# Optimization experiments

Hardware: AMD Instinct MI355X
Metric: run time of the kernel (lower is better)

The kernel has to match this reference:

```python
import jax, jax.numpy as jnp
import numpy as np

# Static problem sizes (uniform complexes so the per-complex torch loop vectorizes)
B, P, L = 8, 512, 64          # complexes, protein atoms/complex, ligand atoms/complex
H, RB = 128, 32               # hidden_dim, radial_bins
CUTOFF = 8.0
NPT, NLT = 20, 16             # atom-type vocab sizes


def _linear_init(k, din, dout):
    s = 1.0 / np.sqrt(din)
    kw, kb = jax.random.split(k)
    W = jax.random.uniform(kw, (din, dout), minval=-s, maxval=s, dtype=jnp.float32)
    b = jax.random.uniform(kb, (dout,), minval=-s, maxval=s, dtype=jnp.float32)
    return W, b


def setup_inputs() -> dict:
    key = jax.random.key(0)
    ks = jax.random.split(key, 12)
    # positions spread over ~a pocket-sized box so the cutoff mask is non-trivial
    protein_pos = jax.random.normal(ks[0], (B * P, 3), dtype=jnp.float32) * 4.0
    ligand_pos = jax.random.normal(ks[1], (B * L, 3), dtype=jnp.float32) * 4.0
    protein_atom_type = jax.random.randint(ks[2], (B * P,), 0, NPT)
    ligand_atom_type = jax.random.randint(ks[3], (B * L,), 0, NLT)
    protein_batch = jnp.repeat(jnp.arange(B), P)
    ligand_batch = jnp.repeat(jnp.arange(B), L)
    prot_emb = jax.random.normal(ks[4], (NPT, H), dtype=jnp.float32)
    lig_emb = jax.random.normal(ks[5], (NLT, H), dtype=jnp.float32)
    W1, b1 = _linear_init(ks[6], 2 * H + RB, H)
    W2, b2 = _linear_init(ks[7], H, H)
    W3, b3 = _linear_init(ks[8], H, H)
    Wr1, br1 = _linear_init(ks[9], H, H)
    Wr2, br2 = _linear_init(ks[10], H, 1)
    return dict(protein_pos=protein_pos, ligand_pos=ligand_pos,
                prot_emb=prot_emb, lig_emb=lig_emb,
                W1=W1, b1=b1, W2=W2, b2=b2, W3=W3, b3=b3,
                Wr1=Wr1, br1=br1, Wr2=Wr2, br2=br2,
                protein_atom_type=protein_atom_type, ligand_atom_type=ligand_atom_type,
                protein_batch=protein_batch, ligand_batch=ligand_batch)


def reference(protein_pos, ligand_pos, prot_emb, lig_emb,
              W1, b1, W2, b2, W3, b3, Wr1, br1, Wr2, br2,
              protein_atom_type, ligand_atom_type, protein_batch, ligand_batch):
    # batches are contiguous with uniform P/L atoms per complex -> reshape to [B, ., .]
    pos_p = protein_pos.reshape(B, P, 3)
    pos_l = ligand_pos.reshape(B, L, 3)
    hp = prot_emb[protein_atom_type].reshape(B, P, H)
    hl = lig_emb[ligand_atom_type].reshape(B, L, H)

    diff = pos_p[:, :, None, :] - pos_l[:, None, :, :]          # [B,P,L,3]
    dist = jnp.linalg.norm(diff, axis=-1)                        # [B,P,L]
    mask = dist < CUTOFF                                         # [B,P,L]

    centers = jnp.linspace(0.0, CUTOFF, RB, dtype=dist.dtype)    # radial_centers buffer
    width = jnp.asarray(0.5 * CUTOFF / RB, dtype=dist.dtype)     # radial_width buffer
    rb = jnp.exp(-0.5 * ((dist[..., None] - centers) / (width + 1e-8)) ** 2)  # [B,P,L,RB]

    pair = jnp.concatenate([
        jnp.broadcast_to(hp[:, :, None, :], (B, P, L, H)),
        jnp.broadcast_to(hl[:, None, :, :], (B, P, L, H)),
        rb,
    ], axis=-1)                                                  # [B,P,L,2H+RB]

    h = jax.nn.relu(pair @ W1 + b1)
    h = jax.nn.relu(h @ W2 + b2)
    h = jax.nn.relu(h @ W3 + b3)                                 # [B,P,L,H]

    m = mask[..., None].astype(h.dtype)
    cnt = jnp.sum(mask, axis=(1, 2)).astype(h.dtype)             # valid pairs per complex
    complex_repr = jnp.sum(h * m, axis=(1, 2)) / jnp.maximum(cnt, 1.0)[:, None]  # [B,H]

    score = jax.nn.relu(complex_repr @ Wr1 + br1) @ Wr2 + br2    # [B,1]
    score = jnp.where(cnt[:, None] > 0, score, 0.0)              # torch emits 0 if no pairs
    return score[:, 0]                                           # [B]
```

## Files before the change

kernel.cpp:

```cpp
#include <hip/hip_runtime.h>
#include <hip/hip_bf16.h>
#include <math.h>

#define NB 8
#define NP 512
#define NL 64
#define NH 128
#define NRB 32
#define NPT 20
#define NLT 16
#define PAIRS_CAP (NP * NL)
#define CHUNKS 512
#define K1 96

typedef __attribute__((ext_vector_type(8))) _Float16 h8;
typedef __attribute__((ext_vector_type(4))) float f4;

__global__ __launch_bounds__(256) void prep(
    const float* __restrict__ ppos, const float* __restrict__ lpos,
    const int* __restrict__ ptype_g, const int* __restrict__ ltype_g,
    const float* __restrict__ pemb, const float* __restrict__ lemb,
    const float* __restrict__ W1, const float* __restrict__ b1,
    const float* __restrict__ W2, const float* __restrict__ W3,
    uint2* __restrict__ rec, unsigned* __restrict__ cnt,
    _Float16* __restrict__ wt1e, _Float16* __restrict__ wt2t,
    _Float16* __restrict__ wt3t, float* __restrict__ acc)
{
  int blk = blockIdx.x, tid = threadIdx.x;

  if (blk < 8) {
    int b = blk;
    int w = tid >> 6, lane = tid & 63;
    __shared__ float slig[NL * 3];
    __shared__ int slt[NL];
    __shared__ unsigned wtot[4];

    if (tid < NL * 3) slig[tid] = lpos[b * NL * 3 + tid];
    if (tid < NL) slt[tid] = ltype_g[b * NL + tid];
    __syncthreads();

    const float* pp = ppos + (size_t)(b * NP + 2 * tid) * 3;
    float p0x = pp[0], p0y = pp[1], p0z = pp[2];
    float p1x = pp[3], p1y = pp[4], p1z = pp[5];
    unsigned pt0 = (unsigned)ptype_g[b * NP + 2 * tid];
    unsigned pt1 = (unsigned)ptype_g[b * NP + 2 * tid + 1];

    unsigned long long m0 = 0ull, m1 = 0ull;
    for (int l = 0; l < NL; ++l) {
      float qx = slig[3 * l + 0], qy = slig[3 * l + 1], qz = slig[3 * l + 2];
      float dx0 = p0x - qx, dy0 = p0y - qy, dz0 = p0z - qz;
      float dx1 = p1x - qx, dy1 = p1y - qy, dz1 = p1z - qz;
      bool v0 = sqrtf(dx0 * dx0 + dy0 * dy0 + dz0 * dz0) < 8.0f;
      bool v1 = sqrtf(dx1 * dx1 + dy1 * dy1 + dz1 * dz1) < 8.0f;
      m0 |= ((unsigned long long)v0) << l;
      m1 |= ((unsigned long long)v1) << l;
    }
    unsigned count = (unsigned)(__popcll(m0) + __popcll(m1));

    unsigned inc = count;
    #pragma unroll
    for (int d = 1; d < 64; d <<= 1) {
      unsigned v = __shfl_up(inc, d);
      if (lane >= d) inc += v;
    }
    if (lane == 63) wtot[w] = inc;
    __syncthreads();
    unsigned wbase = 0;
    for (int i = 0; i < w; ++i) wbase += wtot[i];
    unsigned base = wbase + inc - count;
    if (tid == 255) cnt[b] = wbase + inc;

    uint2* dst = rec + (size_t)b * PAIRS_CAP;
    unsigned long long mm = m0;
    while (mm) {
      int l = __builtin_ctzll(mm); mm &= mm - 1ull;
      float dx = p0x - slig[3 * l], dy = p0y - slig[3 * l + 1], dz = p0z - slig[3 * l + 2];
      float d = sqrtf(dx * dx + dy * dy + dz * dz);
      dst[base++] = (uint2){__float_as_uint(d), (pt0 << 16) | (unsigned)slt[l]};
    }
    mm = m1;
    while (mm) {
      int l = __builtin_ctzll(mm); mm &= mm - 1ull;
      float dx = p1x - slig[3 * l], dy = p1y - slig[3 * l + 1], dz = p1z - slig[3 * l + 2];
      float d = sqrtf(dx * dx + dy * dy + dz * dz);
      dst[base++] = (uint2){__float_as_uint(d), (pt1 << 16) | (unsigned)slt[l]};
    }
    return;
  }

  if (blk == 8) {
    for (int i = tid; i < NB * NH; i += 256) acc[i] = 0.0f;
    return;
  }

  if (blk < 105) {
    int k = blk - 9;
    if (tid >= NH) return;
    int c = tid;
    float v;
    if (k < 32) {
      v = W1[(2 * NH + k) * NH + c];
    } else if (k < 52) {
      int t = k - 32;
      float s = b1[c];
      for (int j = 0; j < NH; ++j)
        s = fmaf(pemb[t * NH + j], W1[j * NH + c], s);
      v = s;
    } else if (k < 68) {
      int t = k - 52;
      float s = 0.0f;
      for (int j = 0; j < NH; ++j)
        s = fmaf(lemb[t * NH + j], W1[(NH + j) * NH + c], s);
      v = s;
    } else {
      v = 0.0f;
    }
    wt1e[c * K1 + k] = (_Float16)v;
    return;
  }

  {
    int k = blk - 105;
    if (tid >= NH) return;
    int c = tid;
    wt2t[c * NH + k] = (_Float16)W2[k * NH + c];
    wt3t[c * NH + k] = (_Float16)W3[k * NH + c];
    return;
  }
}

__device__ __forceinline__ int swz(int row, int col) {
  return row * NH + (col ^ ((row & 7) << 3));
}

__global__ __launch_bounds__(256, 4) void pair_mlp(
    const _Float16* __restrict__ wt1e, const _Float16* __restrict__ wt2t,
    const _Float16* __restrict__ wt3t,
    const float* __restrict__ b2, const float* __restrict__ b3,
    const uint2* __restrict__ rec, const unsigned* __restrict__ cnt,
    float* __restrict__ accum)
{
  __shared__ _Float16 sA[NL * NH];
  __shared__ _Float16 sB[NL * NH];

  int tid = threadIdx.x;
  int cg = __builtin_amdgcn_readfirstlane(tid >> 6);
  int l  = tid & 63;
  int b     = blockIdx.x & 7;
  int chunk = blockIdx.x >> 3;

  unsigned total = cnt[b];
  if ((unsigned)(chunk * 64) >= total) return;

  int idx = chunk * 64 + l;
  int src = ((unsigned)idx < total) ? idx : 0;
  uint2 rcd = rec[(size_t)b * PAIRS_CAP + src];
  float dist = __uint_as_float(rcd.x);
  int pt = (int)(rcd.y >> 16), lt = (int)(rcd.y & 0xffffu);

  const float stepc = 8.0f / 31.0f;
  const float invw = 1.0f / (0.125f + 1e-8f);

  for (int jj = 0; jj < 3; ++jj) {
    int ch = 3 * cg + jj;
    h8 v;
    #pragma unroll
    for (int i = 0; i < 8; ++i) {
      int c = ch * 8 + i;
      float x;
      if (c < 32) { float t = (dist - stepc * (float)c) * invw; x = __expf(-0.5f * t * t); }
      else if (c < 52) x = (c - 32 == pt) ? 1.0f : 0.0f;
      else if (c < 68) x = (c - 52 == lt) ? 1.0f : 0.0f;
      else x = 0.0f;
      v[i] = (_Float16)x;
    }
    *(h8*)&sB[swz(l, ch * 8)] = v;
  }
  __syncthreads();

  int col0 = cg * 32 + (l & 15);
  int krow = 8 * (l >> 4);
  int g4 = (l >> 4) * 4;

  {
    h8 B1[2][3];
    #pragma unroll
    for (int n = 0; n < 2; ++n)
      #pragma unroll
      for (int kk = 0; kk < 3; ++kk)
        B1[n][kk] = *(const h8*)&wt1e[(col0 + 16 * n) * K1 + 32 * kk + krow];

    f4 acc1[4][2];
    #pragma unroll
    for (int m = 0; m < 4; ++m)
      #pragma unroll
      for (int n = 0; n < 2; ++n)
        acc1[m][n] = (f4){0.0f, 0.0f, 0.0f, 0.0f};

    #pragma unroll
    for (int m = 0; m < 4; ++m) {
      int row = 16 * m + (l & 15);
      #pragma unroll
      for (int kk = 0; kk < 3; ++kk) {
        h8 a = *(const h8*)&sB[swz(row, 32 * kk + krow)];
        acc1[m][0] = __builtin_amdgcn_mfma_f32_16x16x32_f16(a, B1[0][kk], acc1[m][0], 0, 0, 0);
        acc1[m][1] = __builtin_amdgcn_mfma_f32_16x16x32_f16(a, B1[1][kk], acc1[m][1], 0, 0, 0);
      }
    }
    #pragma unroll
    for (int m = 0; m < 4; ++m)
      #pragma unroll
      for (int n = 0; n < 2; ++n)
        #pragma unroll
        for (int r = 0; r < 4; ++r) {
          int row = 16 * m + g4 + r;
          sA[swz(row, cg * 32 + 16 * n + (l & 15))] =
              (_Float16)fmaxf(acc1[m][n][r], 0.0f);
        }
  }
  __syncthreads();

  {
    h8 B2[2][4];
    #pragma unroll
    for (int n = 0; n < 2; ++n)
      #pragma unroll
      for (int kk = 0; kk < 4; ++kk)
        B2[n][kk] = *(const h8*)&wt2t[(col0 + 16 * n) * NH + 32 * kk + krow];

    float bias0 = b2[col0], bias1 = b2[col0 + 16];
    f4 acc2[4][2];
    #pragma unroll
    for (int m = 0; m < 4; ++m) {
      acc2[m][0] = (f4){bias0, bias0, bias0, bias0};
      acc2[m][1] = (f4){bias1, bias1, bias1, bias1};
    }
    #pragma unroll
    for (int m = 0; m < 4; ++m) {
      int row = 16 * m + (l & 15);
      #pragma unroll
      for (int kk = 0; kk < 4; ++kk) {
        h8 a = *(const h8*)&sA[swz(row, 32 * kk + krow)];
        acc2[m][0] = __builtin_amdgcn_mfma_f32_16x16x32_f16(a, B2[0][kk], acc2[m][0], 0, 0, 0);
        acc2[m][1] = __builtin_amdgcn_mfma_f32_16x16x32_f16(a, B2[1][kk], acc2[m][1], 0, 0, 0);
      }
    }
    __syncthreads();
    #pragma unroll
    for (int m = 0; m < 4; ++m)
      #pragma unroll
      for (int n = 0; n < 2; ++n)
        #pragma unroll
        for (int r = 0; r < 4; ++r) {
          int row = 16 * m + g4 + r;
          sB[swz(row, cg * 32 + 16 * n + (l & 15))] =
              (_Float16)fmaxf(acc2[m][n][r], 0.0f);
        }
  }
  __syncthreads();

  {
    h8 B3[2][4];
    #pragma unroll
    for (int n = 0; n < 2; ++n)
      #pragma unroll
      for (int kk = 0; kk < 4; ++kk)
        B3[n][kk] = *(const h8*)&wt3t[(col0 + 16 * n) * NH + 32 * kk + krow];

    float bias0 = b3[col0], bias1 = b3[col0 + 16];
    f4 acc3[4][2];
    #pragma unroll
    for (int m = 0; m < 4; ++m) {
      acc3[m][0] = (f4){bias0, bias0, bias0, bias0};
      acc3[m][1] = (f4){bias1, bias1, bias1, bias1};
    }
    #pragma unroll
    for (int m = 0; m < 4; ++m) {
      int row = 16 * m + (l & 15);
      #pragma unroll
      for (int kk = 0; kk < 4; ++kk) {
        h8 a = *(const h8*)&sB[swz(row, 32 * kk + krow)];
        acc3[m][0] = __builtin_amdgcn_mfma_f32_16x16x32_f16(a, B3[0][kk], acc3[m][0], 0, 0, 0);
        acc3[m][1] = __builtin_amdgcn_mfma_f32_16x16x32_f16(a, B3[1][kk], acc3[m][1], 0, 0, 0);
      }
    }

    int rem = (int)total - chunk * 64;
    float cs0 = 0.0f, cs1 = 0.0f;
    #pragma unroll
    for (int m = 0; m < 4; ++m)
      #pragma unroll
      for (int r = 0; r < 4; ++r) {
        int row = 16 * m + g4 + r;
        bool ok = row < rem;
        cs0 += ok ? fmaxf(acc3[m][0][r], 0.0f) : 0.0f;
        cs1 += ok ? fmaxf(acc3[m][1][r], 0.0f) : 0.0f;
      }
    cs0 += __shfl_xor(cs0, 16); cs0 += __shfl_xor(cs0, 32);
    cs1 += __shfl_xor(cs1, 16); cs1 += __shfl_xor(cs1, 32);
    int g = l >> 4;
    if (g == 0)      atomicAdd(&accum[b * NH + cg * 32 + (l & 15)], cs0);
    else if (g == 1) atomicAdd(&accum[b * NH + cg * 32 + 16 + (l & 15)], cs1);
  }
}

__global__ __launch_bounds__(128) void score_head(
    const float* __restrict__ acc, const unsigned* __restrict__ cnt,
    const float* __restrict__ Wr1, const float* __restrict__ br1,
    const float* __restrict__ Wr2, const float* __restrict__ br2,
    float* __restrict__ out)
{
  int b = blockIdx.x;
  int tid = threadIdx.x;
  __shared__ float sr[NH];
  __shared__ float wsum[2];
  unsigned c = cnt[b];
  float denom = fmaxf((float)c, 1.0f);
  sr[tid] = acc[b * NH + tid] / denom;
  __syncthreads();
  float s = br1[tid];
  for (int k = 0; k < NH; ++k)
    s = fmaf(sr[k], Wr1[k * NH + tid], s);
  float v = fmaxf(s, 0.0f) * Wr2[tid];
  #pragma unroll
  for (int d = 1; d < 64; d <<= 1) v += __shfl_xor(v, d);
  if ((tid & 63) == 0) wsum[tid >> 6] = v;
  __syncthreads();
  if (tid == 0)
    out[b] = (c > 0) ? (wsum[0] + wsum[1] + br2[0]) : 0.0f;
}

extern "C" void kernel_launch(void* const* d_in, const int* in_sizes, int n_in,
                              void* d_out, int out_size, void* d_ws, size_t ws_size,
                              hipStream_t stream)
{
  const float* ppos = (const float*)d_in[0];
  const float* lpos = (const float*)d_in[1];
  const float* pemb = (const float*)d_in[2];
  const float* lemb = (const float*)d_in[3];
  const float* W1   = (const float*)d_in[4];
  const float* b1   = (const float*)d_in[5];
  const float* W2   = (const float*)d_in[6];
  const float* b2   = (const float*)d_in[7];
  const float* W3   = (const float*)d_in[8];
  const float* b3   = (const float*)d_in[9];
  const float* Wr1  = (const float*)d_in[10];
  const float* br1  = (const float*)d_in[11];
  const float* Wr2  = (const float*)d_in[12];
  const float* br2  = (const float*)d_in[13];
  const int*   ptyp = (const int*)d_in[14];
  const int*   ltyp = (const int*)d_in[15];

  float* ws  = (float*)d_ws;
  float* acc = ws;
  unsigned* cnt = (unsigned*)(ws + 1024);
  uint2* rec = (uint2*)(ws + 1032);
  _Float16* wt1e = (_Float16*)(ws + 1032 + 524288);
  _Float16* wt2t = (_Float16*)(ws + 1032 + 524288 + 6144);
  _Float16* wt3t = (_Float16*)(ws + 1032 + 524288 + 6144 + 8192);

  prep<<<233, 256, 0, stream>>>(ppos, lpos, ptyp, ltyp, pemb, lemb,
                                W1, b1, W2, W3,
                                rec, cnt, wt1e, wt2t, wt3t, acc);
  pair_mlp<<<NB * CHUNKS, 256, 0, stream>>>(wt1e, wt2t, wt3t, b2, b3,
                                            rec, cnt, acc);
  score_head<<<NB, 128, 0, stream>>>(acc, cnt, Wr1, br1, Wr2, br2, (float*)d_out);
}
```

Measured before the change: 57.72 us.

## Give each wave its own 16-row pair tile, dropping inter-wave barriers

```diff
diff --git a/kernel.cpp b/kernel.cpp
--- a/kernel.cpp
+++ b/kernel.cpp
@@ -130,7 +130,7 @@
 }
 
 __device__ __forceinline__ int swz(int row, int col) {
-  return row * NH + (col ^ ((row & 7) << 3));
+  return row * NH + (col ^ ((row & 15) << 3));
 }
 
 __global__ __launch_bounds__(256, 4) void pair_mlp(
@@ -140,11 +140,11 @@
     const uint2* __restrict__ rec, const unsigned* __restrict__ cnt,
     float* __restrict__ accum)
 {
-  __shared__ _Float16 sA[NL * NH];
-  __shared__ _Float16 sB[NL * NH];
+  __shared__ _Float16 sS[NL * NH];
+  __shared__ float comb[4 * NH];
 
   int tid = threadIdx.x;
-  int cg = __builtin_amdgcn_readfirstlane(tid >> 6);
+  int w  = __builtin_amdgcn_readfirstlane(tid >> 6);
   int l  = tid & 63;
   int b     = blockIdx.x & 7;
   int chunk = blockIdx.x >> 3;
@@ -152,7 +152,11 @@
   unsigned total = cnt[b];
   if ((unsigned)(chunk * 64) >= total) return;
 
-  int idx = chunk * 64 + l;
+  int c16  = l & 15;
+  int g    = l >> 4;
+  int row0 = 16 * w;
+
+  int idx = chunk * 64 + row0 + c16;
   int src = ((unsigned)idx < total) ? idx : 0;
   uint2 rcd = rec[(size_t)b * PAIRS_CAP + src];
   float dist = __uint_as_float(rcd.x);
@@ -161,146 +165,114 @@
   const float stepc = 8.0f / 31.0f;
   const float invw = 1.0f / (0.125f + 1e-8f);
 
-  for (int jj = 0; jj < 3; ++jj) {
-    int ch = 3 * cg + jj;
-    h8 v;
-    #pragma unroll
-    for (int i = 0; i < 8; ++i) {
-      int c = ch * 8 + i;
-      float x;
-      if (c < 32) { float t = (dist - stepc * (float)c) * invw; x = __expf(-0.5f * t * t); }
-      else if (c < 52) x = (c - 32 == pt) ? 1.0f : 0.0f;
-      else if (c < 68) x = (c - 52 == lt) ? 1.0f : 0.0f;
-      else x = 0.0f;
-      v[i] = (_Float16)x;
-    }
-    *(h8*)&sB[swz(l, ch * 8)] = v;
-  }
-  __syncthreads();
-
-  int col0 = cg * 32 + (l & 15);
-  int krow = 8 * (l >> 4);
-  int g4 = (l >> 4) * 4;
+  h8 a1k0, a1k1, a1k2;
+  #pragma unroll
+  for (int j = 0; j < 8; ++j) {
+    int u = 8 * g + j;
+    float t = (dist - stepc * (float)u) * invw;
+    a1k0[j] = (_Float16)__expf(-0.5f * t * t);
+    a1k1[j] = (_Float16)((u < 20) ? ((u == pt) ? 1.0f : 0.0f)
+                                  : ((u - 20 == lt) ? 1.0f : 0.0f));
+    a1k2[j] = (_Float16)(((u < 4) && (u + 12 == lt)) ? 1.0f : 0.0f);
+  }
+
+  f4 acc[8];
+  #pragma unroll
+  for (int nn = 0; nn < 8; ++nn) acc[nn] = (f4){0.0f, 0.0f, 0.0f, 0.0f};
+  #pragma unroll
+  for (int nn = 0; nn < 8; ++nn) {
+    const _Float16* wp = &wt1e[(16 * nn + c16) * K1 + 8 * g];
+    h8 bf0 = *(const h8*)&wp[0];
+    h8 bf1 = *(const h8*)&wp[32];
+    h8 bf2 = *(const h8*)&wp[64];
+    acc[nn] = __builtin_amdgcn_mfma_f32_16x16x32_f16(a1k0, bf0, acc[nn], 0, 0, 0);
+    acc[nn] = __builtin_amdgcn_mfma_f32_16x16x32_f16(a1k1, bf1, acc[nn], 0, 0, 0);
+    acc[nn] = __builtin_amdgcn_mfma_f32_16x16x32_f16(a1k2, bf2, acc[nn], 0, 0, 0);
+  }
+  #pragma unroll
+  for (int nn = 0; nn < 8; ++nn)
+    #pragma unroll
+    for (int r = 0; r < 4; ++r)
+      sS[swz(row0 + 4 * g + r, 16 * nn + c16)] = (_Float16)fmaxf(acc[nn][r], 0.0f);
 
   {
-    h8 B1[2][3];
-    #pragma unroll
-    for (int n = 0; n < 2; ++n)
+    h8 a0 = *(const h8*)&sS[swz(row0 + c16, 8 * g)];
+    h8 a1 = *(const h8*)&sS[swz(row0 + c16, 32 + 8 * g)];
+    h8 a2 = *(const h8*)&sS[swz(row0 + c16, 64 + 8 * g)];
+    h8 a3 = *(const h8*)&sS[swz(row0 + c16, 96 + 8 * g)];
+    f4 acc2[8];
+    #pragma unroll
+    for (int nn = 0; nn < 8; ++nn) {
+      float bb = b2[16 * nn + c16];
+      acc2[nn] = (f4){bb, bb, bb, bb};
+    }
+    #pragma unroll
+    for (int nn = 0; nn < 8; ++nn) {
+      const _Float16* wp = &wt2t[(16 * nn + c16) * NH + 8 * g];
+      h8 bf0 = *(const h8*)&wp[0];
+      h8 bf1 = *(const h8*)&wp[32];
+      h8 bf2 = *(const h8*)&wp[64];
+      h8 bf3 = *(const h8*)&wp[96];
+      acc2[nn] = __builtin_amdgcn_mfma_f32_16x16x32_f16(a0, bf0, acc2[nn], 0, 0, 0);
+      acc2[nn] = __builtin_amdgcn_mfma_f32_16x16x32_f16(a1, bf1, acc2[nn], 0, 0, 0);
+      acc2[nn] = __builtin_amdgcn_mfma_f32_16x16x32_f16(a2, bf2, acc2[nn], 0, 0, 0);
+      acc2[nn] = __builtin_amdgcn_mfma_f32_16x16x32_f16(a3, bf3, acc2[nn], 0, 0, 0);
+    }
+    #pragma unroll
+    for (int nn = 0; nn < 8; ++nn)
       #pragma unroll
-      for (int kk = 0; kk < 3; ++kk)
-        B1[n][kk] = *(const h8*)&wt1e[(col0 + 16 * n) * K1 + 32 * kk + krow];
-
-    f4 acc1[4][2];
-    #pragma unroll
-    for (int m = 0; m < 4; ++m)
-      #pragma unroll
-      for (int n = 0; n < 2; ++n)
-        acc1[m][n] = (f4){0.0f, 0.0f, 0.0f, 0.0f};
-
-    #pragma unroll
-    for (int m = 0; m < 4; ++m) {
-      int row = 16 * m + (l & 15);
-      #pragma unroll
-      for (int kk = 0; kk < 3; ++kk) {
-        h8 a = *(const h8*)&sB[swz(row, 32 * kk + krow)];
-        acc1[m][0] = __builtin_amdgcn_mfma_f32_16x16x32_f16(a, B1[0][kk], acc1[m][0], 0, 0, 0);
-        acc1[m][1] = __builtin_amdgcn_mfma_f32_16x16x32_f16(a, B1[1][kk], acc1[m][1], 0, 0, 0);
-      }
-    }
-    #pragma unroll
-    for (int m = 0; m < 4; ++m)
-      #pragma unroll
-      for (int n = 0; n < 2; ++n)
-        #pragma unroll
-        for (int r = 0; r < 4; ++r) {
-          int row = 16 * m + g4 + r;
-          sA[swz(row, cg * 32 + 16 * n + (l & 15))] =
-              (_Float16)fmaxf(acc1[m][n][r], 0.0f);
-        }
-  }
-  __syncthreads();
-
+      for (int r = 0; r < 4; ++r)
+        sS[swz(row0 + 4 * g + r, 16 * nn + c16)] = (_Float16)fmaxf(acc2[nn][r], 0.0f);
+  }
+
+  float cs[8];
   {
-    h8 B2[2][4];
-    #pragma unroll
-    for (int n = 0; n < 2; ++n)
-      #pragma unroll
-      for (int kk = 0; kk < 4; ++kk)
-        B2[n][kk] = *(const h8*)&wt2t[(col0 + 16 * n) * NH + 32 * kk + krow];
-
-    float bias0 = b2[col0], bias1 = b2[col0 + 16];
-    f4 acc2[4][2];
-    #pragma unroll
-    for (int m = 0; m < 4; ++m) {
-      acc2[m][0] = (f4){bias0, bias0, bias0, bias0};
-      acc2[m][1] = (f4){bias1, bias1, bias1, bias1};
-    }
-    #pragma unroll
-    for (int m = 0; m < 4; ++m) {
-      int row = 16 * m + (l & 15);
-      #pragma unroll
-      for (int kk = 0; kk < 4; ++kk) {
-        h8 a = *(const h8*)&sA[swz(row, 32 * kk + krow)];
-        acc2[m][0] = __builtin_amdgcn_mfma_f32_16x16x32_f16(a, B2[0][kk], acc2[m][0], 0, 0, 0);
-        acc2[m][1] = __builtin_amdgcn_mfma_f32_16x16x32_f16(a, B2[1][kk], acc2[m][1], 0, 0, 0);
-      }
-    }
-    __syncthreads();
-    #pragma unroll
-    for (int m = 0; m < 4; ++m)
-      #pragma unroll
-      for (int n = 0; n < 2; ++n)
-        #pragma unroll
-        for (int r = 0; r < 4; ++r) {
-          int row = 16 * m + g4 + r;
-          sB[swz(row, cg * 32 + 16 * n + (l & 15))] =
-              (_Float16)fmaxf(acc2[m][n][r], 0.0f);
-        }
-  }
-  __syncthreads();
-
-  {
-    h8 B3[2][4];
-    #pragma unroll
-    for (int n = 0; n < 2; ++n)
-      #pragma unroll
-      for (int kk = 0; kk < 4; ++kk)
-        B3[n][kk] = *(const h8*)&wt3t[(col0 + 16 * n) * NH + 32 * kk + krow];
-
-    float bias0 = b3[col0], bias1 = b3[col0 + 16];
-    f4 acc3[4][2];
-    #pragma unroll
-    for (int m = 0; m < 4; ++m) {
-      acc3[m][0] = (f4){bias0, bias0, bias0, bias0};
-      acc3[m][1] = (f4){bias1, bias1, bias1, bias1};
-    }
-    #pragma unroll
-    for (int m = 0; m < 4; ++m) {
-      int row = 16 * m + (l & 15);
-      #pragma unroll
-      for (int kk = 0; kk < 4; ++kk) {
-        h8 a = *(const h8*)&sB[swz(row, 32 * kk + krow)];
-        acc3[m][0] = __builtin_amdgcn_mfma_f32_16x16x32_f16(a, B3[0][kk], acc3[m][0], 0, 0, 0);
-        acc3[m][1] = __builtin_amdgcn_mfma_f32_16x16x32_f16(a, B3[1][kk], acc3[m][1], 0, 0, 0);
-      }
-    }
-
+    h8 a0 = *(const h8*)&sS[swz(row0 + c16, 8 * g)];
+    h8 a1 = *(const h8*)&sS[swz(row0 + c16, 32 + 8 * g)];
+    h8 a2 = *(const h8*)&sS[swz(row0 + c16, 64 + 8 * g)];
+    h8 a3 = *(const h8*)&sS[swz(row0 + c16, 96 + 8 * g)];
+    f4 acc3[8];
+    #pragma unroll
+    for (int nn = 0; nn < 8; ++nn) {
+      float bb = b3[16 * nn + c16];
+      acc3[nn] = (f4){bb, bb, bb, bb};
+    }
+    #pragma unroll
+    for (int nn = 0; nn < 8; ++nn) {
+      const _Float16* wp = &wt3t[(16 * nn + c16) * NH + 8 * g];
+      h8 bf0 = *(const h8*)&wp[0];
+      h8 bf1 = *(const h8*)&wp[32];
+      h8 bf2 = *(const h8*)&wp[64];
+      h8 bf3 = *(const h8*)&wp[96];
+      acc3[nn] = __builtin_amdgcn_mfma_f32_16x16x32_f16(a0, bf0, acc3[nn], 0, 0, 0);
+      acc3[nn] = __builtin_amdgcn_mfma_f32_16x16x32_f16(a1, bf1, acc3[nn], 0, 0, 0);
+      acc3[nn] = __builtin_amdgcn_mfma_f32_16x16x32_f16(a2, bf2, acc3[nn], 0, 0, 0);
+      acc3[nn] = __builtin_amdgcn_mfma_f32_16x16x32_f16(a3, bf3, acc3[nn], 0, 0, 0);
+    }
     int rem = (int)total - chunk * 64;
-    float cs0 = 0.0f, cs1 = 0.0f;
-    #pragma unroll
-    for (int m = 0; m < 4; ++m)
+    #pragma unroll
+    for (int nn = 0; nn < 8; ++nn) {
+      float s = 0.0f;
       #pragma unroll
       for (int r = 0; r < 4; ++r) {
-        int row = 16 * m + g4 + r;
-        bool ok = row < rem;
-        cs0 += ok ? fmaxf(acc3[m][0][r], 0.0f) : 0.0f;
-        cs1 += ok ? fmaxf(acc3[m][1][r], 0.0f) : 0.0f;
+        bool ok = (row0 + 4 * g + r) < rem;
+        s += ok ? fmaxf(acc3[nn][r], 0.0f) : 0.0f;
       }
-    cs0 += __shfl_xor(cs0, 16); cs0 += __shfl_xor(cs0, 32);
-    cs1 += __shfl_xor(cs1, 16); cs1 += __shfl_xor(cs1, 32);
-    int g = l >> 4;
-    if (g == 0)      atomicAdd(&accum[b * NH + cg * 32 + (l & 15)], cs0);
-    else if (g == 1) atomicAdd(&accum[b * NH + cg * 32 + 16 + (l & 15)], cs1);
+      s += __shfl_xor(s, 16);
+      s += __shfl_xor(s, 32);
+      cs[nn] = s;
+    }
+  }
+
+  if (g == 0) {
+    #pragma unroll
+    for (int nn = 0; nn < 8; ++nn)
+      comb[w * NH + 16 * nn + c16] = cs[nn];
+  }
+  __syncthreads();
+  if (tid < NH) {
+    float s = comb[tid] + comb[NH + tid] + comb[2 * NH + tid] + comb[3 * NH + tid];
+    atomicAdd(&accum[b * NH + tid], s);
   }
 }
 
```

Measured after the change: 104.1 us. +80.3%, slower.

## Fuse prep, pair MLP and score head into one cooperative persistent kernel

Applied to the files above, without the earlier changes.

```diff
diff --git a/kernel.cpp b/kernel.cpp
--- a/kernel.cpp
+++ b/kernel.cpp
@@ -1,6 +1,9 @@
 #include <hip/hip_runtime.h>
 #include <hip/hip_bf16.h>
+#include <hip/hip_cooperative_groups.h>
 #include <math.h>
+
+namespace cg = cooperative_groups;
 
 #define NB 8
 #define NP 512
@@ -16,24 +19,37 @@
 typedef __attribute__((ext_vector_type(8))) _Float16 h8;
 typedef __attribute__((ext_vector_type(4))) float f4;
 
-__global__ __launch_bounds__(256) void prep(
+__device__ __forceinline__ int swz(int row, int col) {
+  return row * NH + (col ^ ((row & 7) << 3));
+}
+
+__global__ __launch_bounds__(256, 4) void fused(
     const float* __restrict__ ppos, const float* __restrict__ lpos,
     const int* __restrict__ ptype_g, const int* __restrict__ ltype_g,
     const float* __restrict__ pemb, const float* __restrict__ lemb,
     const float* __restrict__ W1, const float* __restrict__ b1,
-    const float* __restrict__ W2, const float* __restrict__ W3,
+    const float* __restrict__ W2, const float* __restrict__ b2,
+    const float* __restrict__ W3, const float* __restrict__ b3,
+    const float* __restrict__ Wr1, const float* __restrict__ br1,
+    const float* __restrict__ Wr2, const float* __restrict__ br2,
     uint2* __restrict__ rec, unsigned* __restrict__ cnt,
     _Float16* __restrict__ wt1e, _Float16* __restrict__ wt2t,
-    _Float16* __restrict__ wt3t, float* __restrict__ acc)
+    _Float16* __restrict__ wt3t, float* __restrict__ accum,
+    float* __restrict__ out)
 {
-  int blk = blockIdx.x, tid = threadIdx.x;
-
-  if (blk < 8) {
-    int b = blk;
+  __shared__ __align__(16) unsigned char smem[2 * NL * NH * 2];
+  _Float16* sA = (_Float16*)smem;
+  _Float16* sB = (_Float16*)(smem + NL * NH * 2);
+
+  cg::grid_group grid = cg::this_grid();
+  int bid = blockIdx.x, tid = threadIdx.x;
+
+  if (bid < 8) {
+    int b = bid;
     int w = tid >> 6, lane = tid & 63;
-    __shared__ float slig[NL * 3];
-    __shared__ int slt[NL];
-    __shared__ unsigned wtot[4];
+    float* slig = (float*)smem;
+    int* slt = (int*)(smem + 768);
+    unsigned* wtot = (unsigned*)(smem + 1024);
 
     if (tid < NL * 3) slig[tid] = lpos[b * NL * 3 + tid];
     if (tid < NL) slt[tid] = ltype_g[b * NL + tid];
@@ -85,249 +101,230 @@
       float d = sqrtf(dx * dx + dy * dy + dz * dz);
       dst[base++] = (uint2){__float_as_uint(d), (pt1 << 16) | (unsigned)slt[l]};
     }
-    return;
+  } else if (bid == 8) {
+    for (int i = tid; i < NB * NH; i += 256) accum[i] = 0.0f;
+  } else if (bid < 105) {
+    int k = bid - 9;
+    if (tid < NH) {
+      int c = tid;
+      float v;
+      if (k < 32) {
+        v = W1[(2 * NH + k) * NH + c];
+      } else if (k < 52) {
+        int t = k - 32;
+        float s = b1[c];
+        for (int j = 0; j < NH; ++j)
+          s = fmaf(pemb[t * NH + j], W1[j * NH + c], s);
+        v = s;
+      } else if (k < 68) {
+        int t = k - 52;
+        float s = 0.0f;
+        for (int j = 0; j < NH; ++j)
+          s = fmaf(lemb[t * NH + j], W1[(NH + j) * NH + c], s);
+        v = s;
+      } else {
+        v = 0.0f;
+      }
+      wt1e[c * K1 + k] = (_Float16)v;
+    }
+  } else if (bid < 233) {
+    int k = bid - 105;
+    if (tid < NH) {
+      int c = tid;
+      wt2t[c * NH + k] = (_Float16)W2[k * NH + c];
+      wt3t[c * NH + k] = (_Float16)W3[k * NH + c];
+    }
   }
 
-  if (blk == 8) {
-    for (int i = tid; i < NB * NH; i += 256) acc[i] = 0.0f;
-    return;
+  grid.sync();
+
+  {
+    int cg_w = __builtin_amdgcn_readfirstlane(tid >> 6);
+    int l  = tid & 63;
+    int col0 = cg_w * 32 + (l & 15);
+    int krow = 8 * (l >> 4);
+    int g4 = (l >> 4) * 4;
+    const float stepc = 8.0f / 31.0f;
+    const float invw = 1.0f / (0.125f + 1e-8f);
+
+    for (int v = bid; v < NB * CHUNKS; v += gridDim.x) {
+      int b = v & 7;
+      int chunk = v >> 3;
+      unsigned total = cnt[b];
+      if ((unsigned)(chunk * 64) >= total) continue;
+
+      __syncthreads();
+
+      int idx = chunk * 64 + l;
+      int src = ((unsigned)idx < total) ? idx : 0;
+      uint2 rcd = rec[(size_t)b * PAIRS_CAP + src];
+      float dist = __uint_as_float(rcd.x);
+      int pt = (int)(rcd.y >> 16), lt = (int)(rcd.y & 0xffffu);
+
+      for (int jj = 0; jj < 3; ++jj) {
+        int ch = 3 * cg_w + jj;
+        h8 vv;
+        #pragma unroll
+        for (int i = 0; i < 8; ++i) {
+          int c = ch * 8 + i;
+          float x;
+          if (c < 32) { float t = (dist - stepc * (float)c) * invw; x = __expf(-0.5f * t * t); }
+          else if (c < 52) x = (c - 32 == pt) ? 1.0f : 0.0f;
+          else if (c < 68) x = (c - 52 == lt) ? 1.0f : 0.0f;
+          else x = 0.0f;
+          vv[i] = (_Float16)x;
+        }
+        *(h8*)&sB[swz(l, ch * 8)] = vv;
+      }
+      __syncthreads();
+
+      {
+        h8 B1[2][3];
+        #pragma unroll
+        for (int n = 0; n < 2; ++n)
+          #pragma unroll
+          for (int kk = 0; kk < 3; ++kk)
+            B1[n][kk] = *(const h8*)&wt1e[(col0 + 16 * n) * K1 + 32 * kk + krow];
+
+        f4 acc1[4][2];
+        #pragma unroll
+        for (int m = 0; m < 4; ++m)
+          #pragma unroll
+          for (int n = 0; n < 2; ++n)
+            acc1[m][n] = (f4){0.0f, 0.0f, 0.0f, 0.0f};
+
+        #pragma unroll
+        for (int m = 0; m < 4; ++m) {
+          int row = 16 * m + (l & 15);
+          #pragma unroll
+          for (int kk = 0; kk < 3; ++kk) {
+            h8 a = *(const h8*)&sB[swz(row, 32 * kk + krow)];
+            acc1[m][0] = __builtin_amdgcn_mfma_f32_16x16x32_f16(a, B1[0][kk], acc1[m][0], 0, 0, 0);
+            acc1[m][1] = __builtin_amdgcn_mfma_f32_16x16x32_f16(a, B1[1][kk], acc1[m][1], 0, 0, 0);
+          }
+        }
+        #pragma unroll
+        for (int m = 0; m < 4; ++m)
+          #pragma unroll
+          for (int n = 0; n < 2; ++n)
+            #pragma unroll
+            for (int r = 0; r < 4; ++r) {
+              int row = 16 * m + g4 + r;
+              sA[swz(row, cg_w * 32 + 16 * n + (l & 15))] =
+                  (_Float16)fmaxf(acc1[m][n][r], 0.0f);
+            }
+      }
+      __syncthreads();
+
+      {
+        h8 B2[2][4];
+        #pragma unroll
+        for (int n = 0; n < 2; ++n)
+          #pragma unroll
+          for (int kk = 0; kk < 4; ++kk)
+            B2[n][kk] = *(const h8*)&wt2t[(col0 + 16 * n) * NH + 32 * kk + krow];
+
+        float bias0 = b2[col0], bias1 = b2[col0 + 16];
+        f4 acc2[4][2];
+        #pragma unroll
+        for (int m = 0; m < 4; ++m) {
+          acc2[m][0] = (f4){bias0, bias0, bias0, bias0};
+          acc2[m][1] = (f4){bias1, bias1, bias1, bias1};
+        }
+        #pragma unroll
+        for (int m = 0; m < 4; ++m) {
+          int row = 16 * m + (l & 15);
+          #pragma unroll
+          for (int kk = 0; kk < 4; ++kk) {
+            h8 a = *(const h8*)&sA[swz(row, 32 * kk + krow)];
+            acc2[m][0] = __builtin_amdgcn_mfma_f32_16x16x32_f16(a, B2[0][kk], acc2[m][0], 0, 0, 0);
+            acc2[m][1] = __builtin_amdgcn_mfma_f32_16x16x32_f16(a, B2[1][kk], acc2[m][1], 0, 0, 0);
+          }
+        }
+        __syncthreads();
+        #pragma unroll
+        for (int m = 0; m < 4; ++m)
+          #pragma unroll
+          for (int n = 0; n < 2; ++n)
+            #pragma unroll
+            for (int r = 0; r < 4; ++r) {
+              int row = 16 * m + g4 + r;
+              sB[swz(row, cg_w * 32 + 16 * n + (l & 15))] =
+                  (_Float16)fmaxf(acc2[m][n][r], 0.0f);
+            }
+      }
+      __syncthreads();
+
+      {
+        h8 B3[2][4];
+        #pragma unroll
+        for (int n = 0; n < 2; ++n)
+          #pragma unroll
+          for (int kk = 0; kk < 4; ++kk)
+            B3[n][kk] = *(const h8*)&wt3t[(col0 + 16 * n) * NH + 32 * kk + krow];
+
+        float bias0 = b3[col0], bias1 = b3[col0 + 16];
+        f4 acc3[4][2];
+        #pragma unroll
+        for (int m = 0; m < 4; ++m) {
+          acc3[m][0] = (f4){bias0, bias0, bias0, bias0};
+          acc3[m][1] = (f4){bias1, bias1, bias1, bias1};
+        }
+        #pragma unroll
+        for (int m = 0; m < 4; ++m) {
+          int row = 16 * m + (l & 15);
+          #pragma unroll
+          for (int kk = 0; kk < 4; ++kk) {
+            h8 a = *(const h8*)&sB[swz(row, 32 * kk + krow)];
+            acc3[m][0] = __builtin_amdgcn_mfma_f32_16x16x32_f16(a, B3[0][kk], acc3[m][0], 0, 0, 0);
+            acc3[m][1] = __builtin_amdgcn_mfma_f32_16x16x32_f16(a, B3[1][kk], acc3[m][1], 0, 0, 0);
+          }
+        }
+
+        int rem = (int)total - chunk * 64;
+        float cs0 = 0.0f, cs1 = 0.0f;
+        #pragma unroll
+        for (int m = 0; m < 4; ++m)
+          #pragma unroll
+          for (int r = 0; r < 4; ++r) {
+            int row = 16 * m + g4 + r;
+            bool ok = row < rem;
+            cs0 += ok ? fmaxf(acc3[m][0][r], 0.0f) : 0.0f;
+            cs1 += ok ? fmaxf(acc3[m][1][r], 0.0f) : 0.0f;
+          }
+        cs0 += __shfl_xor(cs0, 16); cs0 += __shfl_xor(cs0, 32);
+        cs1 += __shfl_xor(cs1, 16); cs1 += __shfl_xor(cs1, 32);
+        int g = l >> 4;
+        if (g == 0)      atomicAdd(&accum[b * NH + cg_w * 32 + (l & 15)], cs0);
+        else if (g == 1) atomicAdd(&accum[b * NH + cg_w * 32 + 16 + (l & 15)], cs1);
+      }
+    }
   }
 
-  if (blk < 105) {
-    int k = blk - 9;
-    if (tid >= NH) return;
-    int c = tid;
-    float v;
-    if (k < 32) {
-      v = W1[(2 * NH + k) * NH + c];
-    } else if (k < 52) {
-      int t = k - 32;
-      float s = b1[c];
-      for (int j = 0; j < NH; ++j)
-        s = fmaf(pemb[t * NH + j], W1[j * NH + c], s);
-      v = s;
-    } else if (k < 68) {
-      int t = k - 52;
-      float s = 0.0f;
-      for (int j = 0; j < NH; ++j)
-        s = fmaf(lemb[t * NH + j], W1[(NH + j) * NH + c], s);
-      v = s;
-    } else {
-      v = 0.0f;
-    }
-    wt1e[c * K1 + k] = (_Float16)v;
-    return;
+  grid.sync();
+
+  if (bid < NB) {
+    int b = bid;
+    float* sr = (float*)smem;
+    float* wsum = (float*)(smem + 512);
+    unsigned c = cnt[b];
+    float denom = fmaxf((float)c, 1.0f);
+    if (tid < NH) sr[tid] = accum[b * NH + tid] / denom;
+    __syncthreads();
+    float vv = 0.0f;
+    if (tid < NH) {
+      float s = br1[tid];
+      for (int k = 0; k < NH; ++k)
+        s = fmaf(sr[k], Wr1[k * NH + tid], s);
+      vv = fmaxf(s, 0.0f) * Wr2[tid];
+    }
+    #pragma unroll
+    for (int d = 1; d < 64; d <<= 1) vv += __shfl_xor(vv, d);
+    if ((tid & 63) == 0) wsum[tid >> 6] = vv;
+    __syncthreads();
+    if (tid == 0)
+      out[b] = (c > 0) ? (wsum[0] + wsum[1] + br2[0]) : 0.0f;
   }
-
-  {
-    int k = blk - 105;
-    if (tid >= NH) return;
-    int c = tid;
-    wt2t[c * NH + k] = (_Float16)W2[k * NH + c];
-    wt3t[c * NH + k] = (_Float16)W3[k * NH + c];
-    return;
-  }
-}
-
-__device__ __forceinline__ int swz(int row, int col) {
-  return row * NH + (col ^ ((row & 7) << 3));
-}
-
-__global__ __launch_bounds__(256, 4) void pair_mlp(
-    const _Float16* __restrict__ wt1e, const _Float16* __restrict__ wt2t,
-    const _Float16* __restrict__ wt3t,
-    const float* __restrict__ b2, const float* __restrict__ b3,
-    const uint2* __restrict__ rec, const unsigned* __restrict__ cnt,
-    float* __restrict__ accum)
-{
-  __shared__ _Float16 sA[NL * NH];
-  __shared__ _Float16 sB[NL * NH];
-
-  int tid = threadIdx.x;
-  int cg = __builtin_amdgcn_readfirstlane(tid >> 6);
-  int l  = tid & 63;
-  int b     = blockIdx.x & 7;
-  int chunk = blockIdx.x >> 3;
-
-  unsigned total = cnt[b];
-  if ((unsigned)(chunk * 64) >= total) return;
-
-  int idx = chunk * 64 + l;
-  int src = ((unsigned)idx < total) ? idx : 0;
-  uint2 rcd = rec[(size_t)b * PAIRS_CAP + src];
-  float dist = __uint_as_float(rcd.x);
-  int pt = (int)(rcd.y >> 16), lt = (int)(rcd.y & 0xffffu);
-
-  const float stepc = 8.0f / 31.0f;
-  const float invw = 1.0f / (0.125f + 1e-8f);
-
-  for (int jj = 0; jj < 3; ++jj) {
-    int ch = 3 * cg + jj;
-    h8 v;
-    #pragma unroll
-    for (int i = 0; i < 8; ++i) {
-      int c = ch * 8 + i;
-      float x;
-      if (c < 32) { float t = (dist - stepc * (float)c) * invw; x = __expf(-0.5f * t * t); }
-      else if (c < 52) x = (c - 32 == pt) ? 1.0f : 0.0f;
-      else if (c < 68) x = (c - 52 == lt) ? 1.0f : 0.0f;
-      else x = 0.0f;
-      v[i] = (_Float16)x;
-    }
-    *(h8*)&sB[swz(l, ch * 8)] = v;
-  }
-  __syncthreads();
-
-  int col0 = cg * 32 + (l & 15);
-  int krow = 8 * (l >> 4);
-  int g4 = (l >> 4) * 4;
-
-  {
-    h8 B1[2][3];
-    #pragma unroll
-    for (int n = 0; n < 2; ++n)
-      #pragma unroll
-      for (int kk = 0; kk < 3; ++kk)
-        B1[n][kk] = *(const h8*)&wt1e[(col0 + 16 * n) * K1 + 32 * kk + krow];
-
-    f4 acc1[4][2];
-    #pragma unroll
-    for (int m = 0; m < 4; ++m)
-      #pragma unroll
-      for (int n = 0; n < 2; ++n)
-        acc1[m][n] = (f4){0.0f, 0.0f, 0.0f, 0.0f};
-
-    #pragma unroll
-    for (int m = 0; m < 4; ++m) {
-      int row = 16 * m + (l & 15);
-      #pragma unroll
-      for (int kk = 0; kk < 3; ++kk) {
-        h8 a = *(const h8*)&sB[swz(row, 32 * kk + krow)];
-        acc1[m][0] = __builtin_amdgcn_mfma_f32_16x16x32_f16(a, B1[0][kk], acc1[m][0], 0, 0, 0);
-        acc1[m][1] = __builtin_amdgcn_mfma_f32_16x16x32_f16(a, B1[1][kk], acc1[m][1], 0, 0, 0);
-      }
-    }
-    #pragma unroll
-    for (int m = 0; m < 4; ++m)
-      #pragma unroll
-      for (int n = 0; n < 2; ++n)
-        #pragma unroll
-        for (int r = 0; r < 4; ++r) {
-          int row = 16 * m + g4 + r;
-          sA[swz(row, cg * 32 + 16 * n + (l & 15))] =
-              (_Float16)fmaxf(acc1[m][n][r], 0.0f);
-        }
-  }
-  __syncthreads();
-
-  {
-    h8 B2[2][4];
-    #pragma unroll
-    for (int n = 0; n < 2; ++n)
-      #pragma unroll
-      for (int kk = 0; kk < 4; ++kk)
-        B2[n][kk] = *(const h8*)&wt2t[(col0 + 16 * n) * NH + 32 * kk + krow];
-
-    float bias0 = b2[col0], bias1 = b2[col0 + 16];
-    f4 acc2[4][2];
-    #pragma unroll
-    for (int m = 0; m < 4; ++m) {
-      acc2[m][0] = (f4){bias0, bias0, bias0, bias0};
-      acc2[m][1] = (f4){bias1, bias1, bias1, bias1};
-    }
-    #pragma unroll
-    for (int m = 0; m < 4; ++m) {
-      int row = 16 * m + (l & 15);
-      #pragma unroll
-      for (int kk = 0; kk < 4; ++kk) {
-        h8 a = *(const h8*)&sA[swz(row, 32 * kk + krow)];
-        acc2[m][0] = __builtin_amdgcn_mfma_f32_16x16x32_f16(a, B2[0][kk], acc2[m][0], 0, 0, 0);
-        acc2[m][1] = __builtin_amdgcn_mfma_f32_16x16x32_f16(a, B2[1][kk], acc2[m][1], 0, 0, 0);
-      }
-    }
-    __syncthreads();
-    #pragma unroll
-    for (int m = 0; m < 4; ++m)
-      #pragma unroll
-      for (int n = 0; n < 2; ++n)
-        #pragma unroll
-        for (int r = 0; r < 4; ++r) {
-          int row = 16 * m + g4 + r;
-          sB[swz(row, cg * 32 + 16 * n + (l & 15))] =
-              (_Float16)fmaxf(acc2[m][n][r], 0.0f);
-        }
-  }
-  __syncthreads();
-
-  {
-    h8 B3[2][4];
-    #pragma unroll
-    for (int n = 0; n < 2; ++n)
-      #pragma unroll
-      for (int kk = 0; kk < 4; ++kk)
-        B3[n][kk] = *(const h8*)&wt3t[(col0 + 16 * n) * NH + 32 * kk + krow];
-
-    float bias0 = b3[col0], bias1 = b3[col0 + 16];
-    f4 acc3[4][2];
-    #pragma unroll
-    for (int m = 0; m < 4; ++m) {
-      acc3[m][0] = (f4){bias0, bias0, bias0, bias0};
-      acc3[m][1] = (f4){bias1, bias1, bias1, bias1};
-    }
-    #pragma unroll
-    for (int m = 0; m < 4; ++m) {
-      int row = 16 * m + (l & 15);
-      #pragma unroll
-      for (int kk = 0; kk < 4; ++kk) {
-        h8 a = *(const h8*)&sB[swz(row, 32 * kk + krow)];
-        acc3[m][0] = __builtin_amdgcn_mfma_f32_16x16x32_f16(a, B3[0][kk], acc3[m][0], 0, 0, 0);
-        acc3[m][1] = __builtin_amdgcn_mfma_f32_16x16x32_f16(a, B3[1][kk], acc3[m][1], 0, 0, 0);
-      }
-    }
-
-    int rem = (int)total - chunk * 64;
-    float cs0 = 0.0f, cs1 = 0.0f;
-    #pragma unroll
-    for (int m = 0; m < 4; ++m)
-      #pragma unroll
-      for (int r = 0; r < 4; ++r) {
-        int row = 16 * m + g4 + r;
-        bool ok = row < rem;
-        cs0 += ok ? fmaxf(acc3[m][0][r], 0.0f) : 0.0f;
-        cs1 += ok ? fmaxf(acc3[m][1][r], 0.0f) : 0.0f;
-      }
-    cs0 += __shfl_xor(cs0, 16); cs0 += __shfl_xor(cs0, 32);
-    cs1 += __shfl_xor(cs1, 16); cs1 += __shfl_xor(cs1, 32);
-    int g = l >> 4;
-    if (g == 0)      atomicAdd(&accum[b * NH + cg * 32 + (l & 15)], cs0);
-    else if (g == 1) atomicAdd(&accum[b * NH + cg * 32 + 16 + (l & 15)], cs1);
-  }
-}
-
-__global__ __launch_bounds__(128) void score_head(
-    const float* __restrict__ acc, const unsigned* __restrict__ cnt,
-    const float* __restrict__ Wr1, const float* __restrict__ br1,
-    const float* __restrict__ Wr2, const float* __restrict__ br2,
-    float* __restrict__ out)
-{
-  int b = blockIdx.x;
-  int tid = threadIdx.x;
-  __shared__ float sr[NH];
-  __shared__ float wsum[2];
-  unsigned c = cnt[b];
-  float denom = fmaxf((float)c, 1.0f);
-  sr[tid] = acc[b * NH + tid] / denom;
-  __syncthreads();
-  float s = br1[tid];
-  for (int k = 0; k < NH; ++k)
-    s = fmaf(sr[k], Wr1[k * NH + tid], s);
-  float v = fmaxf(s, 0.0f) * Wr2[tid];
-  #pragma unroll
-  for (int d = 1; d < 64; d <<= 1) v += __shfl_xor(v, d);
-  if ((tid & 63) == 0) wsum[tid >> 6] = v;
-  __syncthreads();
-  if (tid == 0)
-    out[b] = (c > 0) ? (wsum[0] + wsum[1] + br2[0]) : 0.0f;
 }
 
 extern "C" void kernel_launch(void* const* d_in, const int* in_sizes, int n_in,
@@ -358,11 +355,24 @@
   _Float16* wt1e = (_Float16*)(ws + 1032 + 524288);
   _Float16* wt2t = (_Float16*)(ws + 1032 + 524288 + 6144);
   _Float16* wt3t = (_Float16*)(ws + 1032 + 524288 + 6144 + 8192);
-
-  prep<<<233, 256, 0, stream>>>(ppos, lpos, ptyp, ltyp, pemb, lemb,
-                                W1, b1, W2, W3,
-                                rec, cnt, wt1e, wt2t, wt3t, acc);
-  pair_mlp<<<NB * CHUNKS, 256, 0, stream>>>(wt1e, wt2t, wt3t, b2, b3,
-                                            rec, cnt, acc);
-  score_head<<<NB, 128, 0, stream>>>(acc, cnt, Wr1, br1, Wr2, br2, (float*)d_out);
+  float* outp = (float*)d_out;
+
+  int perCU = 0;
+  hipError_t e = hipOccupancyMaxActiveBlocksPerMultiprocessor(
+      &perCU, (const void*)fused, 256, 0);
+  if (e != hipSuccess || perCU < 1) perCU = 1;
+  int grid = perCU * 256;
+  if (grid > 1024) grid = 1024;
+  if (grid < 233) grid = 233;
+
+  void* args[] = {
+    (void*)&ppos, (void*)&lpos, (void*)&ptyp, (void*)&ltyp,
+    (void*)&pemb, (void*)&lemb, (void*)&W1, (void*)&b1,
+    (void*)&W2, (void*)&b2, (void*)&W3, (void*)&b3,
+    (void*)&Wr1, (void*)&br1, (void*)&Wr2, (void*)&br2,
+    (void*)&rec, (void*)&cnt, (void*)&wt1e, (void*)&wt2t,
+    (void*)&wt3t, (void*)&acc, (void*)&outp
+  };
+  hipLaunchCooperativeKernel((const void*)fused, dim3(grid), dim3(256),
+                             args, 0, stream);
 }
```

Measured after the change: 200.0 us. +246.5%, slower.
